# Optimization experiments

Hardware: AMD Instinct MI355X
Metric: run time of the kernel (lower is better)

## Reference

```python
import jax, jax.numpy as jnp
import numpy as np

EPS = 1e-5
HD = 16          # hidden_dim
OC = 256         # out_chs
NH = 8           # num_heads (groups of qkv conv)
DV = OC // (2 * HD)  # per-head value dim = 8


def conv_bn_silu(x, w, gamma, beta, mean, var, stride=1, pad=1, groups=1):
    # Conv2d(bias=False) + BatchNorm2d(eval) + SiLU, NCHW/OIHW
    y = jax.lax.conv_general_dilated(
        x, w, (stride, stride), [(pad, pad), (pad, pad)],
        dimension_numbers=('NCHW', 'OIHW', 'NCHW'),
        feature_group_count=groups)
    inv = gamma * jax.lax.rsqrt(var + EPS)
    y = y * inv[None, :, None, None] + (beta - mean * inv)[None, :, None, None]
    return y * jax.nn.sigmoid(y)


def _bn_params(key, c):
    k1, k2, k3, k4 = jax.random.split(key, 4)
    g = 1.0 + 0.1 * jax.random.normal(k1, (c,), jnp.float32)
    b = 0.1 * jax.random.normal(k2, (c,), jnp.float32)
    m = 0.1 * jax.random.normal(k3, (c,), jnp.float32)
    v = jax.random.uniform(k4, (c,), jnp.float32, 0.5, 1.5)
    return g, b, m, v


def setup_inputs() -> dict:
    key = jax.random.key(0)
    ks = jax.random.split(key, 8)
    B, C, H, W = 16, 256, 80, 80
    qkv_out = HD * 2 + OC // 2  # 160
    d = {}
    d['x'] = jax.random.normal(ks[0], (B, C, H, W), jnp.float32)
    # qkv_conv: grouped 3x3, groups=NH -> in per group = C//NH
    d['qkv_w'] = jax.random.normal(ks[1], (qkv_out, C // NH, 3, 3), jnp.float32) * 0.05
    d['qkv_g'], d['qkv_b'], d['qkv_m'], d['qkv_v'] = _bn_params(ks[2], qkv_out)
    # hidden_conv: dense 3x3
    d['hid_w'] = jax.random.normal(ks[3], (OC, C, 3, 3), jnp.float32) * 0.02
    d['hid_g'], d['hid_b'], d['hid_m'], d['hid_v'] = _bn_params(ks[4], OC)
    # out_conv: 1x1 on (OC//2*3) channels
    d['out_w'] = jax.random.normal(ks[5], (OC, OC // 2 * 3, 1, 1), jnp.float32) * 0.05
    d['out_g'], d['out_b'], d['out_m'], d['out_v'] = _bn_params(ks[6], OC)
    return d


def reference(x, qkv_w, qkv_g, qkv_b, qkv_m, qkv_v,
              hid_w, hid_g, hid_b, hid_m, hid_v,
              out_w, out_g, out_b, out_m, out_v):
    B, C, H, W = x.shape
    N = H * W
    qkv = conv_bn_silu(x, qkv_w, qkv_g, qkv_b, qkv_m, qkv_v, stride=1, pad=1, groups=NH)
    q = qkv[:, :HD]               # (B, HD, H, W)
    k = qkv[:, HD:2 * HD]
    v = qkv[:, 2 * HD:]           # (B, OC//2, H, W)
    # permute to (B, N, HD) / (B, N, HD, DV), channel-major reshape matches torch .view
    q = q.transpose(0, 2, 3, 1).reshape(B, N, HD)
    k = k.transpose(0, 2, 3, 1).reshape(B, N, HD)
    v = v.transpose(0, 2, 3, 1).reshape(B, N, HD, DV)
    # per-pixel tiny attention: attn[b,n,i,j] = softmax_j(q_i * k_j)
    attn = jax.nn.softmax(q[..., :, None] * k[..., None, :], axis=-1)  # (B,N,HD,HD)
    y = jnp.einsum('bnij,bnjd->bnid', attn, v)                          # (B,N,HD,DV)
    # torch: permute(0,2,3,1).view(B, OC//2, H, W)
    y = y.transpose(0, 2, 3, 1).reshape(B, OC // 2, H, W)
    h = conv_bn_silu(x, hid_w, hid_g, hid_b, hid_m, hid_v, stride=1, pad=1)
    y = jnp.concatenate([y, h], axis=1)  # (B, OC//2*3, H, W)
    return conv_bn_silu(y, out_w, out_g, out_b, out_m, out_v, stride=1, pad=0)
```

## Files before the change

kernel.cpp:

```cpp
#include <hip/hip_runtime.h>
#include <stdint.h>

typedef unsigned short u16;
typedef unsigned int u32;
typedef __attribute__((ext_vector_type(4))) float f32x4;
typedef __attribute__((ext_vector_type(8))) __bf16 bf16x8;

#define EPS_BN 1e-5f

__device__ __forceinline__ u16 f2bf(float f) {
  u32 u = __builtin_bit_cast(u32, f);
  u32 r = (u + 0x7fffu + ((u >> 16) & 1u)) >> 16;
  return (u16)r;
}

__device__ __forceinline__ float silu_f(float v) {
  return v / (1.0f + __expf(-v));
}

__device__ __forceinline__ void gll16(const void* g, void* l) {
  __builtin_amdgcn_global_load_lds(
      (__attribute__((address_space(1))) void*)(void*)g,
      (__attribute__((address_space(3))) void*)l, 16, 0, 0);
}

__global__ __launch_bounds__(256) void prep(
    const float* __restrict__ qkv_w, const float* __restrict__ qg,
    const float* __restrict__ qb, const float* __restrict__ qm,
    const float* __restrict__ qv,
    const float* __restrict__ hid_w, const float* __restrict__ hg,
    const float* __restrict__ hb, const float* __restrict__ hm,
    const float* __restrict__ hv,
    const float* __restrict__ out_w, const float* __restrict__ og,
    const float* __restrict__ ob, const float* __restrict__ om,
    const float* __restrict__ ov,
    u16* __restrict__ wtb, u16* __restrict__ w2b, u16* __restrict__ wqp,
    float* __restrict__ bnq_s, float* __restrict__ bnq_b,
    float* __restrict__ bnh_s, float* __restrict__ bnh_b,
    float* __restrict__ bn2s, float* __restrict__ bn2b,
    float* __restrict__ zpg)
{
  const int gid = blockIdx.x * 256 + threadIdx.x;
  if (gid < 256 * 2304) {
    int j = gid / 2304, k = gid - j * 2304;
    int tap = k >> 8, c = k & 255;
    wtb[gid] = f2bf(hid_w[(j * 256 + c) * 9 + tap]);
  }
  if (gid < 73728) {
    int g = gid / 9216;
    int r = gid - g * 9216;
    int j = r / 288, k = r - j * 288;
    int tap = k >> 5, cg = k & 31;
    float v = 0.f;
    if (j < 20) v = qkv_w[((g * 20 + j) * 32 + cg) * 9 + tap];
    wqp[gid] = f2bf(v);
  }
  if (gid < 98304) w2b[gid] = f2bf(out_w[gid]);
  if (gid < 160) {
    float iv = qg[gid] * rsqrtf(qv[gid] + EPS_BN);
    bnq_s[gid] = iv; bnq_b[gid] = qb[gid] - qm[gid] * iv;
  }
  if (gid < 256) {
    float iv = hg[gid] * rsqrtf(hv[gid] + EPS_BN);
    bnh_s[gid] = iv; bnh_b[gid] = hb[gid] - hm[gid] * iv;
    float iv2 = og[gid] * rsqrtf(ov[gid] + EPS_BN);
    bn2s[gid] = iv2; bn2b[gid] = ob[gid] - om[gid] * iv2;
  }
  if (gid < 64) zpg[gid] = 0.f;
}

__global__ __launch_bounds__(256) void nchw2nhwc(
    const float* __restrict__ x, u16* __restrict__ xn)
{
  __shared__ u16 T[80 * 66];
  const int t = threadIdx.x;
  const int ct = blockIdx.x;
  const int h  = blockIdx.y;
  const int b  = blockIdx.z;
  const float* src = x + ((size_t)b * 256 + ct * 64) * 6400 + h * 80;
  for (int it = 0; it < 5; ++it) {
    int idx = it * 256 + t;
    int cl = idx / 20, w4 = idx - cl * 20;
    float4 v = *(const float4*)(src + (size_t)cl * 6400 + w4 * 4);
    T[(w4 * 4 + 0) * 66 + cl] = f2bf(v.x);
    T[(w4 * 4 + 1) * 66 + cl] = f2bf(v.y);
    T[(w4 * 4 + 2) * 66 + cl] = f2bf(v.z);
    T[(w4 * 4 + 3) * 66 + cl] = f2bf(v.w);
  }
  __syncthreads();
  u16* dst = xn + ((size_t)(b * 80 + h) * 80) * 256 + ct * 64;
  for (int it = 0; it < 5; ++it) {
    int idx = it * 256 + t;
    int wl = idx >> 4;
    int cl = (idx & 15) * 4;
    ushort4 v4;
    v4.x = T[wl * 66 + cl + 0];
    v4.y = T[wl * 66 + cl + 1];
    v4.z = T[wl * 66 + cl + 2];
    v4.w = T[wl * 66 + cl + 3];
    *(ushort4*)(dst + (size_t)wl * 256 + cl) = v4;
  }
}

__global__ __launch_bounds__(512, 4) void gemm_main(
    const u16* __restrict__ xn, const u16* __restrict__ wt,
    const float* __restrict__ bns, const float* __restrict__ bnb,
    const float* __restrict__ zpg, u16* __restrict__ ycat)
{
  __shared__ __attribute__((aligned(16))) u16 Al[128 * 64];
  __shared__ __attribute__((aligned(16))) u16 Bl[256 * 64];
  const int t = threadIdx.x;
  const int wave = t >> 6, lane = t & 63;
  const int wm = wave >> 2;
  const int wn = wave & 3;
  const int orig = blockIdx.x;
  const int wg = (orig & 7) * 100 + (orig >> 3);
  const int ptile = wg * 128;

  const int srcc = (((lane & 7) ^ ((lane >> 3) & 7)) * 8);
  const int c16 = lane & 15, lq = lane >> 4;

  int pbA[2], hhA[2], wwA[2];
#pragma unroll
  for (int l = 0; l < 2; ++l) {
    int row = wave * 8 + (lane >> 3) + l * 64;
    int p = ptile + row;
    pbA[l] = p;
    int hw = p % 6400;
    hhA[l] = hw / 80;
    wwA[l] = hw - (hw / 80) * 80;
  }
  int bofB[4];
#pragma unroll
  for (int l = 0; l < 4; ++l) {
    int row = wave * 8 + (lane >> 3) + l * 64;
    bofB[l] = row * 2304 + srcc;
  }

  f32x4 acc[4][4];
#pragma unroll
  for (int m = 0; m < 4; ++m)
#pragma unroll
    for (int n = 0; n < 4; ++n) {
      f32x4 z = {0.f, 0.f, 0.f, 0.f};
      acc[m][n] = z;
    }

  for (int ks = 0; ks < 36; ++ks) {
    const int k0 = ks * 64;
    const int tap = ks >> 2;
    const int c0 = (ks & 3) * 64;
    const int dh = tap / 3 - 1, dw = tap - (tap / 3) * 3 - 1;
    const int dp = dh * 80 + dw;
    __syncthreads();
#pragma unroll
    for (int l = 0; l < 2; ++l) {
      bool ok = ((unsigned)(hhA[l] + dh) < 80u) & ((unsigned)(wwA[l] + dw) < 80u);
      const u16* src = ok
          ? (xn + ((size_t)(pbA[l] + dp) * 256 + c0 + srcc))
          : (const u16*)zpg;
      gll16(src, Al + (wave * 8 + l * 64) * 64);
    }
#pragma unroll
    for (int l = 0; l < 4; ++l)
      gll16(wt + (size_t)(bofB[l] + k0), Bl + (wave * 8 + l * 64) * 64);
    __syncthreads();
#pragma unroll
    for (int kk = 0; kk < 2; ++kk) {
      const int q = kk * 4 + lq;
      bf16x8 av[4], bv[4];
#pragma unroll
      for (int m = 0; m < 4; ++m) {
        int r = wm * 64 + m * 16 + c16;
        av[m] = *(const bf16x8*)(Al + r * 64 + (q ^ (r & 7)) * 8);
      }
#pragma unroll
      for (int n = 0; n < 4; ++n) {
        int j = wn * 64 + n * 16 + c16;
        bv[n] = *(const bf16x8*)(Bl + j * 64 + (q ^ (j & 7)) * 8);
      }
#pragma unroll
      for (int m = 0; m < 4; ++m)
#pragma unroll
        for (int n = 0; n < 4; ++n)
          acc[m][n] = __builtin_amdgcn_mfma_f32_16x16x32_bf16(
              av[m], bv[n], acc[m][n], 0, 0, 0);
    }
  }

  const int rg = lq;
#pragma unroll
  for (int n = 0; n < 4; ++n) {
    int j = wn * 64 + n * 16 + c16;
    float sc = bns[j], bi = bnb[j];
#pragma unroll
    for (int m = 0; m < 4; ++m) {
      int p0 = ptile + wm * 64 + m * 16 + rg * 4;
#pragma unroll
      for (int r = 0; r < 4; ++r) {
        float v = silu_f(acc[m][n][r] * sc + bi);
        ycat[(size_t)(p0 + r) * 384 + 128 + j] = f2bf(v);
      }
    }
  }
}

__global__ __launch_bounds__(256, 2) void qkv_attn(
    const u16* __restrict__ xn, const u16* __restrict__ wqp,
    const float* __restrict__ bnq_s, const float* __restrict__ bnq_b,
    u16* __restrict__ ycat)
{
  __shared__ __attribute__((aligned(16))) char LB[81920];
  u16* HB0 = (u16*)LB;
  u16* HB1 = (u16*)(LB + 40960);
  float* qs = (float*)LB;

  const int t = threadIdx.x;
  const int wave = t >> 6, lane = t & 63;
  const int orig = blockIdx.x;
  const int wg = (orig & 7) * 100 + (orig >> 3);
  const int ptile = wg * 128;
  const int pbase = ptile - 88;

  const int srcc = (((lane & 7) ^ ((lane >> 3) & 7)) * 8);
  const int q = lane >> 4, c16 = lane & 15;

  int ph[2], pw[2];
#pragma unroll
  for (int m = 0; m < 2; ++m) {
    int p = ptile + wave * 32 + m * 16 + c16;
    int hw = p % 6400;
    ph[m] = hw / 80;
    pw[m] = hw - (hw / 80) * 80;
  }

  auto STAGE_H = [&](int cc, u16* dst) {
#pragma unroll
    for (int r = 0; r < 10; ++r) {
      int row = r * 32 + wave * 8 + (lane >> 3);
      int p = pbase + row;
      int pc = p < 0 ? 0 : (p > 102399 ? 102399 : p);
      gll16(xn + (size_t)pc * 256 + cc * 64 + srcc,
            dst + (r * 32 + wave * 8) * 64);
    }
  };

  bf16x8 zv;
#pragma unroll
  for (int i = 0; i < 8; ++i) zv[i] = (__bf16)0.0f;

  f32x4 acc[2][16];
#pragma unroll
  for (int m = 0; m < 2; ++m)
#pragma unroll
    for (int f = 0; f < 16; ++f) {
      f32x4 z = {0.f, 0.f, 0.f, 0.f};
      acc[m][f] = z;
    }

  STAGE_H(0, HB0);
  asm volatile("s_waitcnt vmcnt(0)" ::: "memory");
  __builtin_amdgcn_sched_barrier(0);
  __syncthreads();

#pragma unroll
  for (int cc = 0; cc < 4; ++cc) {
    const u16* HBc = (cc & 1) ? HB1 : HB0;
    u16* HBn = (cc & 1) ? HB0 : HB1;
    if (cc < 3) STAGE_H(cc + 1, HBn);
    for (int tap = 0; tap < 9; ++tap) {
      const int dh = tap / 3 - 1, dw = tap - (tap / 3) * 3 - 1;
      const int dp = dh * 80 + dw;
      bf16x8 bq[2][2];
#pragma unroll
      for (int h = 0; h < 2; ++h)
#pragma unroll
        for (int nf = 0; nf < 2; ++nf) {
          int row = (2 * cc + h) * 32 + nf * 16 + c16;
          bq[h][nf] =
              *(const bf16x8*)(wqp + (size_t)row * 288 + tap * 32 + q * 8);
        }
      bf16x8 av[2][2];
#pragma unroll
      for (int m = 0; m < 2; ++m) {
        int rl = wave * 32 + m * 16 + c16 + 88 + dp;
        bool ok = ((unsigned)(ph[m] + dh) < 80u) &
                  ((unsigned)(pw[m] + dw) < 80u);
#pragma unroll
        for (int h = 0; h < 2; ++h) {
          int q8 = h * 4 + q;
          bf16x8 raw = *(const bf16x8*)(HBc + rl * 64 + ((q8 ^ (rl & 7)) * 8));
          av[m][h] = ok ? raw : zv;
        }
      }
#pragma unroll
      for (int h = 0; h < 2; ++h)
#pragma unroll
        for (int m = 0; m < 2; ++m)
#pragma unroll
          for (int nf = 0; nf < 2; ++nf)
            acc[m][(2 * cc + h) * 2 + nf] = __builtin_amdgcn_mfma_f32_16x16x32_bf16(
                av[m][h], bq[h][nf], acc[m][(2 * cc + h) * 2 + nf], 0, 0, 0);
    }
    if (cc < 3) {
      asm volatile("s_waitcnt vmcnt(0)" ::: "memory");
      __builtin_amdgcn_sched_barrier(0);
      __syncthreads();
    }
  }

  asm volatile("s_waitcnt vmcnt(0)" ::: "memory");
  __builtin_amdgcn_sched_barrier(0);
  __syncthreads();

#pragma unroll
  for (int f = 0; f < 16; ++f) {
    int jj = (f & 1) * 16 + c16;
    if (jj >= 20) continue;
    int oc = (f >> 1) * 20 + jj;
    float sc = bnq_s[oc], bi = bnq_b[oc];
#pragma unroll
    for (int m = 0; m < 2; ++m) {
      int pl0 = wave * 32 + m * 16 + q * 4;
#pragma unroll
      for (int r = 0; r < 4; ++r)
        qs[(pl0 + r) * 160 + oc] = silu_f(acc[m][f][r] * sc + bi);
    }
  }
  __syncthreads();

  for (int it = 0; it < 8; ++it) {
    int idx = it * 256 + t;
    int px = idx >> 4, i = idx & 15;
    const float* row = qs + px * 160;
    const float qi = row[i];
    float s[16];
    float mx = -3.4e38f;
#pragma unroll
    for (int j = 0; j < 16; ++j) { s[j] = qi * row[16 + j]; mx = fmaxf(mx, s[j]); }
    float sum = 0.f;
#pragma unroll
    for (int j = 0; j < 16; ++j) { s[j] = __expf(s[j] - mx); sum += s[j]; }
    const float inv = 1.0f / sum;
    float y[8];
#pragma unroll
    for (int d = 0; d < 8; ++d) y[d] = 0.f;
#pragma unroll
    for (int j = 0; j < 16; ++j) {
      const float a = s[j];
      const float* vr = row + 32 + j * 8;
#pragma unroll
      for (int d = 0; d < 8; ++d) y[d] += a * vr[d];
    }
    union { u16 u[8]; uint4 v4; } pk;
#pragma unroll
    for (int d = 0; d < 8; ++d) pk.u[d] = f2bf(y[d] * inv);
    *(uint4*)(ycat + (size_t)(ptile + px) * 384 + i * 8) = pk.v4;
  }
}

__global__ __launch_bounds__(512, 4) void gemm_out(
    const u16* __restrict__ w2, const u16* __restrict__ ycat,
    const float* __restrict__ bns, const float* __restrict__ bnb,
    float* __restrict__ out)
{
  __shared__ __attribute__((aligned(16))) u16 Al[256 * 64];
  __shared__ __attribute__((aligned(16))) u16 Bl[128 * 64];
  const int t = threadIdx.x;
  const int wave = t >> 6, lane = t & 63;
  const int wm = wave >> 1;
  const int wn = wave & 1;
  const int orig = blockIdx.x;
  const int wg = (orig & 7) * 100 + (orig >> 3);
  const int ptile = wg * 128;

  const int srcc = (((lane & 7) ^ ((lane >> 3) & 7)) * 8);
  const int c16 = lane & 15, lq = lane >> 4;

  int bofA[4], bofB[2];
#pragma unroll
  for (int l = 0; l < 4; ++l) {
    int row = wave * 8 + (lane >> 3) + l * 64;
    bofA[l] = row * 384 + srcc;
  }
#pragma unroll
  for (int l = 0; l < 2; ++l) {
    int row = wave * 8 + (lane >> 3) + l * 64;
    bofB[l] = (ptile + row) * 384 + srcc;
  }

  f32x4 acc[4][4];
#pragma unroll
  for (int m = 0; m < 4; ++m)
#pragma unroll
    for (int n = 0; n < 4; ++n) {
      f32x4 z = {0.f, 0.f, 0.f, 0.f};
      acc[m][n] = z;
    }

  for (int ks = 0; ks < 6; ++ks) {
    const int k0 = ks * 64;
    __syncthreads();
#pragma unroll
    for (int l = 0; l < 4; ++l)
      gll16(w2 + (size_t)(bofA[l] + k0), Al + (wave * 8 + l * 64) * 64);
#pragma unroll
    for (int l = 0; l < 2; ++l)
      gll16(ycat + (size_t)(bofB[l] + k0), Bl + (wave * 8 + l * 64) * 64);
    __syncthreads();
#pragma unroll
    for (int kk = 0; kk < 2; ++kk) {
      const int q = kk * 4 + lq;
      bf16x8 av[4], bv[4];
#pragma unroll
      for (int m = 0; m < 4; ++m) {
        int r = wm * 64 + m * 16 + c16;
        av[m] = *(const bf16x8*)(Al + r * 64 + (q ^ (r & 7)) * 8);
      }
#pragma unroll
      for (int n = 0; n < 4; ++n) {
        int j = wn * 64 + n * 16 + c16;
        bv[n] = *(const bf16x8*)(Bl + j * 64 + (q ^ (j & 7)) * 8);
      }
#pragma unroll
      for (int m = 0; m < 4; ++m)
#pragma unroll
        for (int n = 0; n < 4; ++n)
          acc[m][n] = __builtin_amdgcn_mfma_f32_16x16x32_bf16(
              av[m], bv[n], acc[m][n], 0, 0, 0);
    }
  }

  const int rg = lq;
  const int b = ptile / 6400;
  const int hwb = ptile - b * 6400;
#pragma unroll
  for (int m = 0; m < 4; ++m) {
    int oc0 = wm * 64 + m * 16 + rg * 4;
#pragma unroll
    for (int n = 0; n < 4; ++n) {
      int hw = hwb + wn * 64 + n * 16 + c16;
#pragma unroll
      for (int r = 0; r < 4; ++r) {
        int oc = oc0 + r;
        float v = silu_f(acc[m][n][r] * bns[oc] + bnb[oc]);
        out[((size_t)b * 256 + oc) * 6400 + hw] = v;
      }
    }
  }
}

extern "C" void kernel_launch(void* const* d_in, const int* in_sizes, int n_in,
                              void* d_out, int out_size, void* d_ws, size_t ws_size,
                              hipStream_t stream) {
  (void)in_sizes; (void)n_in; (void)out_size; (void)ws_size;
  const float* x    = (const float*)d_in[0];
  const float* qkvw = (const float*)d_in[1];
  const float* qg   = (const float*)d_in[2];
  const float* qb   = (const float*)d_in[3];
  const float* qm   = (const float*)d_in[4];
  const float* qv   = (const float*)d_in[5];
  const float* hw_  = (const float*)d_in[6];
  const float* hg   = (const float*)d_in[7];
  const float* hb   = (const float*)d_in[8];
  const float* hm   = (const float*)d_in[9];
  const float* hv   = (const float*)d_in[10];
  const float* ow   = (const float*)d_in[11];
  const float* og   = (const float*)d_in[12];
  const float* ob   = (const float*)d_in[13];
  const float* om   = (const float*)d_in[14];
  const float* ov   = (const float*)d_in[15];

  char* ws = (char*)d_ws;
  float* zpg   = (float*)(ws + 0);
  float* bnq_s = (float*)(ws + 256);
  float* bnq_b = (float*)(ws + 1280);
  float* bnh_s = (float*)(ws + 2304);
  float* bnh_b = (float*)(ws + 3328);
  float* bn2s  = (float*)(ws + 4352);
  float* bn2b  = (float*)(ws + 5376);
  u16*   wtb   = (u16*)(ws + 6400);
  u16*   w2b   = (u16*)(ws + 1186048);
  u16*   wqp   = (u16*)(ws + 1382656);
  u16*   xn    = (u16*)(ws + 1536000);
  u16*   ycat  = (u16*)(ws + 119500800);
  float* out   = (float*)d_out;

  prep<<<dim3(2304), dim3(256), 0, stream>>>(
      qkvw, qg, qb, qm, qv, hw_, hg, hb, hm, hv, ow, og, ob, om, ov,
      wtb, w2b, wqp, bnq_s, bnq_b, bnh_s, bnh_b, bn2s, bn2b, zpg);
  nchw2nhwc<<<dim3(4, 80, 16), dim3(256), 0, stream>>>(x, xn);
  gemm_main<<<dim3(800), dim3(512), 0, stream>>>(
      xn, wtb, bnh_s, bnh_b, zpg, ycat);
  qkv_attn<<<dim3(800), dim3(256), 0, stream>>>(
      xn, wqp, bnq_s, bnq_b, ycat);
  gemm_out<<<dim3(800), dim3(512), 0, stream>>>(
      w2b, ycat, bn2s, bn2b, out);
}
```

Baseline: 313.2 us.

## Shrink LDS in qkv_attn and split gemm_out into smaller output tiles

qkv_attn drops its double-buffered LDS staging for a single 40KB buffer that is loaded synchronously, and processes the attention epilogue in two 64-pixel halves so the fp32 staging fits that buffer. Launch bounds are raised to 3 blocks per CU to increase occupancy. gemm_out goes from 512-thread blocks covering all 256 output channels to 256-thread blocks covering 128 channels on a 2x800 grid, halving LDS per block. The cost is lost load/compute overlap in qkv_attn and the B tile being loaded twice in gemm_out.

```diff
diff --git a/kernel.cpp b/kernel.cpp
--- a/kernel.cpp
+++ b/kernel.cpp
@@ -205,14 +205,13 @@
   }
 }
 
-__global__ __launch_bounds__(256, 2) void qkv_attn(
+__global__ __launch_bounds__(256, 3) void qkv_attn(
     const u16* __restrict__ xn, const u16* __restrict__ wqp,
     const float* __restrict__ bnq_s, const float* __restrict__ bnq_b,
     u16* __restrict__ ycat)
 {
-  __shared__ __attribute__((aligned(16))) char LB[81920];
-  u16* HB0 = (u16*)LB;
-  u16* HB1 = (u16*)(LB + 40960);
+  __shared__ __attribute__((aligned(16))) char LB[40960];
+  u16* HB = (u16*)LB;
   float* qs = (float*)LB;
 
   const int t = threadIdx.x;
@@ -234,14 +233,14 @@
     pw[m] = hw - (hw / 80) * 80;
   }
 
-  auto STAGE_H = [&](int cc, u16* dst) {
+  auto STAGE_H = [&](int cc) {
 #pragma unroll
     for (int r = 0; r < 10; ++r) {
       int row = r * 32 + wave * 8 + (lane >> 3);
       int p = pbase + row;
       int pc = p < 0 ? 0 : (p > 102399 ? 102399 : p);
       gll16(xn + (size_t)pc * 256 + cc * 64 + srcc,
-            dst + (r * 32 + wave * 8) * 64);
+            HB + (r * 32 + wave * 8) * 64);
     }
   };
 
@@ -258,16 +257,11 @@
       acc[m][f] = z;
     }
 
-  STAGE_H(0, HB0);
-  asm volatile("s_waitcnt vmcnt(0)" ::: "memory");
-  __builtin_amdgcn_sched_barrier(0);
-  __syncthreads();
-
 #pragma unroll
   for (int cc = 0; cc < 4; ++cc) {
-    const u16* HBc = (cc & 1) ? HB1 : HB0;
-    u16* HBn = (cc & 1) ? HB0 : HB1;
-    if (cc < 3) STAGE_H(cc + 1, HBn);
+    __syncthreads();
+    STAGE_H(cc);
+    __syncthreads();
     for (int tap = 0; tap < 9; ++tap) {
       const int dh = tap / 3 - 1, dw = tap - (tap / 3) * 3 - 1;
       const int dp = dh * 80 + dw;
@@ -289,7 +283,7 @@
 #pragma unroll
         for (int h = 0; h < 2; ++h) {
           int q8 = h * 4 + q;
-          bf16x8 raw = *(const bf16x8*)(HBc + rl * 64 + ((q8 ^ (rl & 7)) * 8));
+          bf16x8 raw = *(const bf16x8*)(HB + rl * 64 + ((q8 ^ (rl & 7)) * 8));
           av[m][h] = ok ? raw : zv;
         }
       }
@@ -302,92 +296,86 @@
             acc[m][(2 * cc + h) * 2 + nf] = __builtin_amdgcn_mfma_f32_16x16x32_bf16(
                 av[m][h], bq[h][nf], acc[m][(2 * cc + h) * 2 + nf], 0, 0, 0);
     }
-    if (cc < 3) {
-      asm volatile("s_waitcnt vmcnt(0)" ::: "memory");
-      __builtin_amdgcn_sched_barrier(0);
-      __syncthreads();
-    }
-  }
-
-  asm volatile("s_waitcnt vmcnt(0)" ::: "memory");
-  __builtin_amdgcn_sched_barrier(0);
+  }
+
   __syncthreads();
 
 #pragma unroll
-  for (int f = 0; f < 16; ++f) {
-    int jj = (f & 1) * 16 + c16;
-    if (jj >= 20) continue;
-    int oc = (f >> 1) * 20 + jj;
-    float sc = bnq_s[oc], bi = bnq_b[oc];
-#pragma unroll
-    for (int m = 0; m < 2; ++m) {
-      int pl0 = wave * 32 + m * 16 + q * 4;
-#pragma unroll
-      for (int r = 0; r < 4; ++r)
-        qs[(pl0 + r) * 160 + oc] = silu_f(acc[m][f][r] * sc + bi);
-    }
-  }
-  __syncthreads();
-
-  for (int it = 0; it < 8; ++it) {
-    int idx = it * 256 + t;
-    int px = idx >> 4, i = idx & 15;
-    const float* row = qs + px * 160;
-    const float qi = row[i];
-    float s[16];
-    float mx = -3.4e38f;
-#pragma unroll
-    for (int j = 0; j < 16; ++j) { s[j] = qi * row[16 + j]; mx = fmaxf(mx, s[j]); }
-    float sum = 0.f;
-#pragma unroll
-    for (int j = 0; j < 16; ++j) { s[j] = __expf(s[j] - mx); sum += s[j]; }
-    const float inv = 1.0f / sum;
-    float y[8];
-#pragma unroll
-    for (int d = 0; d < 8; ++d) y[d] = 0.f;
-#pragma unroll
-    for (int j = 0; j < 16; ++j) {
-      const float a = s[j];
-      const float* vr = row + 32 + j * 8;
-#pragma unroll
-      for (int d = 0; d < 8; ++d) y[d] += a * vr[d];
-    }
-    union { u16 u[8]; uint4 v4; } pk;
-#pragma unroll
-    for (int d = 0; d < 8; ++d) pk.u[d] = f2bf(y[d] * inv);
-    *(uint4*)(ycat + (size_t)(ptile + px) * 384 + i * 8) = pk.v4;
-  }
-}
-
-__global__ __launch_bounds__(512, 4) void gemm_out(
+  for (int hf = 0; hf < 2; ++hf) {
+    if ((wave >> 1) == hf) {
+#pragma unroll
+      for (int f = 0; f < 16; ++f) {
+        int jj = (f & 1) * 16 + c16;
+        if (jj >= 20) continue;
+        int oc = (f >> 1) * 20 + jj;
+        float sc = bnq_s[oc], bi = bnq_b[oc];
+#pragma unroll
+        for (int m = 0; m < 2; ++m) {
+          int pl0 = (wave & 1) * 32 + m * 16 + q * 4;
+#pragma unroll
+          for (int r = 0; r < 4; ++r)
+            qs[(pl0 + r) * 160 + oc] = silu_f(acc[m][f][r] * sc + bi);
+        }
+      }
+    }
+    __syncthreads();
+    for (int it = 0; it < 4; ++it) {
+      int idx = it * 256 + t;
+      int pxl = idx >> 4, i = idx & 15;
+      const float* row = qs + pxl * 160;
+      const float qi = row[i];
+      float s[16];
+      float mx = -3.4e38f;
+#pragma unroll
+      for (int j = 0; j < 16; ++j) { s[j] = qi * row[16 + j]; mx = fmaxf(mx, s[j]); }
+      float sum = 0.f;
+#pragma unroll
+      for (int j = 0; j < 16; ++j) { s[j] = __expf(s[j] - mx); sum += s[j]; }
+      const float inv = 1.0f / sum;
+      float y[8];
+#pragma unroll
+      for (int d = 0; d < 8; ++d) y[d] = 0.f;
+#pragma unroll
+      for (int j = 0; j < 16; ++j) {
+        const float a = s[j];
+        const float* vr = row + 32 + j * 8;
+#pragma unroll
+        for (int d = 0; d < 8; ++d) y[d] += a * vr[d];
+      }
+      union { u16 u[8]; uint4 v4; } pk;
+#pragma unroll
+      for (int d = 0; d < 8; ++d) pk.u[d] = f2bf(y[d] * inv);
+      *(uint4*)(ycat + (size_t)(ptile + hf * 64 + pxl) * 384 + i * 8) = pk.v4;
+    }
+    __syncthreads();
+  }
+}
+
+__global__ __launch_bounds__(256, 2) void gemm_out(
     const u16* __restrict__ w2, const u16* __restrict__ ycat,
     const float* __restrict__ bns, const float* __restrict__ bnb,
     float* __restrict__ out)
 {
-  __shared__ __attribute__((aligned(16))) u16 Al[256 * 64];
+  __shared__ __attribute__((aligned(16))) u16 Al[128 * 64];
   __shared__ __attribute__((aligned(16))) u16 Bl[128 * 64];
   const int t = threadIdx.x;
   const int wave = t >> 6, lane = t & 63;
-  const int wm = wave >> 1;
-  const int wn = wave & 1;
-  const int orig = blockIdx.x;
-  const int wg = (orig & 7) * 100 + (orig >> 3);
-  const int ptile = wg * 128;
+  const int wr = wave >> 1, wc = wave & 1;
+  const int orig = blockIdx.y * 2 + blockIdx.x;
+  const int wg = (orig & 7) * 200 + (orig >> 3);
+  const int octile = (wg / 800) * 128;
+  const int ptile = (wg % 800) * 128;
 
   const int srcc = (((lane & 7) ^ ((lane >> 3) & 7)) * 8);
-  const int c16 = lane & 15, lq = lane >> 4;
-
-  int bofA[4], bofB[2];
-#pragma unroll
-  for (int l = 0; l < 4; ++l) {
-    int row = wave * 8 + (lane >> 3) + l * 64;
-    bofA[l] = row * 384 + srcc;
-  }
-#pragma unroll
-  for (int l = 0; l < 2; ++l) {
-    int row = wave * 8 + (lane >> 3) + l * 64;
-    bofB[l] = (ptile + row) * 384 + srcc;
-  }
+  int bofA[4], bofB[4];
+#pragma unroll
+  for (int c = 0; c < 4; ++c) {
+    int m = wave * 32 + c * 8 + (lane >> 3);
+    bofA[c] = (octile + m) * 384 + srcc;
+    bofB[c] = (ptile + m) * 384 + srcc;
+  }
+  u16* AlW = Al + wave * 2048;
+  u16* BlW = Bl + wave * 2048;
 
   f32x4 acc[4][4];
 #pragma unroll
@@ -402,25 +390,24 @@
     const int k0 = ks * 64;
     __syncthreads();
 #pragma unroll
-    for (int l = 0; l < 4; ++l)
-      gll16(w2 + (size_t)(bofA[l] + k0), Al + (wave * 8 + l * 64) * 64);
-#pragma unroll
-    for (int l = 0; l < 2; ++l)
-      gll16(ycat + (size_t)(bofB[l] + k0), Bl + (wave * 8 + l * 64) * 64);
+    for (int c = 0; c < 4; ++c) gll16(w2 + (size_t)(bofA[c] + k0), AlW + c * 512);
+#pragma unroll
+    for (int c = 0; c < 4; ++c) gll16(ycat + (size_t)(bofB[c] + k0), BlW + c * 512);
     __syncthreads();
 #pragma unroll
     for (int kk = 0; kk < 2; ++kk) {
-      const int q = kk * 4 + lq;
+      const int q = kk * 4 + (lane >> 4);
+      const int c16 = lane & 15;
       bf16x8 av[4], bv[4];
 #pragma unroll
       for (int m = 0; m < 4; ++m) {
-        int r = wm * 64 + m * 16 + c16;
+        int r = wr * 64 + m * 16 + c16;
         av[m] = *(const bf16x8*)(Al + r * 64 + (q ^ (r & 7)) * 8);
       }
 #pragma unroll
       for (int n = 0; n < 4; ++n) {
-        int j = wn * 64 + n * 16 + c16;
-        bv[n] = *(const bf16x8*)(Bl + j * 64 + (q ^ (j & 7)) * 8);
+        int r = wc * 64 + n * 16 + c16;
+        bv[n] = *(const bf16x8*)(Bl + r * 64 + (q ^ (r & 7)) * 8);
       }
 #pragma unroll
       for (int m = 0; m < 4; ++m)
@@ -431,15 +418,15 @@
     }
   }
 
-  const int rg = lq;
+  const int c16 = lane & 15, rg = lane >> 4;
   const int b = ptile / 6400;
   const int hwb = ptile - b * 6400;
 #pragma unroll
   for (int m = 0; m < 4; ++m) {
-    int oc0 = wm * 64 + m * 16 + rg * 4;
+    int oc0 = octile + wr * 64 + m * 16 + rg * 4;
 #pragma unroll
     for (int n = 0; n < 4; ++n) {
-      int hw = hwb + wn * 64 + n * 16 + c16;
+      int hw = hwb + wc * 64 + n * 16 + c16;
 #pragma unroll
       for (int r = 0; r < 4; ++r) {
         int oc = oc0 + r;
@@ -494,6 +481,6 @@
       xn, wtb, bnh_s, bnh_b, zpg, ycat);
   qkv_attn<<<dim3(800), dim3(256), 0, stream>>>(
       xn, wqp, bnq_s, bnq_b, ycat);
-  gemm_out<<<dim3(800), dim3(512), 0, stream>>>(
+  gemm_out<<<dim3(2, 800), dim3(256), 0, stream>>>(
       w2b, ycat, bn2s, bn2b, out);
 }
```

New measurement: 336.9 us. 1.08x slower.
